# Performance work log

Measured on AMD Instinct MI355X. Metric: run time of the kernel, lower is better.

Reference implementation:

```python
import jax, jax.numpy as jnp
import numpy as np

B, CIN, COUT, K, IH, IW = 2, 32, 32, 9, 256, 256
OH, OW = 512, 512


def setup_inputs() -> dict:
    key = jax.random.key(0)
    k0, k1, k2, k3 = jax.random.split(key, 4)
    stdv = 1.0 / np.sqrt(CIN * K)
    x = jax.random.normal(k0, (B, CIN, IH, IW), jnp.float32)
    weight = jax.random.uniform(k1, (CIN, COUT, K), jnp.float32, -stdv, stdv)
    bias = jax.random.uniform(k2, (COUT,), jnp.float32, -stdv, stdv)
    # continuous (x, y) coords into the OUTPUT plane; keep strictly inside so x0+1/y0+1 are valid
    sm = jax.random.uniform(k3, (IH, IW, K, 2), jnp.float32)
    scale = jnp.array([(OW - 1) * 0.999, (OH - 1) * 0.999], jnp.float32)
    sample_map = sm * scale
    return {"x": x, "weight": weight, "bias": bias, "sample_map": sample_map, "oh": OH, "ow": OW}


def reference(x, weight, bias, sample_map, oh, ow):
    Bb, Cin, Ih, Iw = x.shape
    Cout = weight.shape[1]
    Kk = weight.shape[2]
    P = Ih * Iw
    xf = x.reshape(Bb, Cin, P)
    # per-kernel-tap weight transform of every input pixel: [B, Cout, K, P]
    contrib = jnp.einsum('bip,iok->bokp', xf, weight)

    sx = sample_map[..., 0].reshape(P, Kk).T  # [K, P] x-coords in output
    sy = sample_map[..., 1].reshape(P, Kk).T  # [K, P] y-coords in output
    x0f = jnp.floor(sx)
    y0f = jnp.floor(sy)
    dx = sx - x0f
    dy = sy - y0f
    x0 = jnp.clip(x0f.astype(jnp.int32), 0, ow - 1)
    y0 = jnp.clip(y0f.astype(jnp.int32), 0, oh - 1)
    x1 = jnp.clip(x0 + 1, 0, ow - 1)
    y1 = jnp.clip(y0 + 1, 0, oh - 1)

    # bilinear splat weights and flat output indices for the 4 corners: [4, K, P]
    w = jnp.stack([(1 - dx) * (1 - dy), dx * (1 - dy), (1 - dx) * dy, dx * dy], 0)
    idx = jnp.stack([y0 * ow + x0, y0 * ow + x1, y1 * ow + x0, y1 * ow + x1], 0)

    vals = contrib[:, :, None, :, :] * w[None, None, :, :, :]  # [B, Cout, 4, K, P]
    out = jnp.zeros((Bb, Cout, oh * ow), vals.dtype).at[:, :, idx].add(vals)
    return out.reshape(Bb, Cout, oh, ow) + bias[None, :, None, None]
```

## Files before the change

### kernel.cpp

```cpp
#include <hip/hip_runtime.h>
#include <hip/hip_fp16.h>

#define CIN 32
#define COUT 32
#define KK 9
#define PIX 65536
#define OH 512
#define OW 512
#define OHOW (OH*OW)
#define NCH 64
#define TW 16
#define TH 4
#define TPX (TW*TH)
#define NTX (OW/TW)
#define NTY (OH/TH)
#define NTILE (NTX*NTY)
#define NBIN NTILE
#define NPK (PIX*KK)
#define NSEG 4
#define SCAP 96
#define CAPT (NSEG*SCAP)

#define OFF_CNT 0
#define OFF_WT  (256*1024)
#define OFF_ENT (512*1024)
#define OFF_CB  (OFF_ENT + (size_t)NBIN*NSEG*SCAP*8)
#define WS_NEED (OFF_CB + (size_t)NPK*NCH*2)

typedef __bf16    bf16x8 __attribute__((ext_vector_type(8)));
typedef _Float16  f16x8  __attribute__((ext_vector_type(8)));
typedef float     f32x4  __attribute__((ext_vector_type(4)));

__device__ __forceinline__ unsigned short f2h(float v)
{
    return __half_as_ushort(__float2half_rn(v));
}

__device__ __forceinline__ void corners(float sx, float sy,
    int& x0, int& y0, int& x1, int& y1, float& dx, float& dy)
{
    const float x0f = floorf(sx), y0f = floorf(sy);
    dx = sx - x0f; dy = sy - y0f;
    x0 = min(max((int)x0f, 0), OW - 1);
    y0 = min(max((int)y0f, 0), OH - 1);
    x1 = min(x0 + 1, OW - 1);
    y1 = min(y0 + 1, OH - 1);
}

__global__ __launch_bounds__(256) void k_wtb(
    const float* __restrict__ w, __bf16* __restrict__ wth, __bf16* __restrict__ wtl)
{
    const int t = blockIdx.x * 256 + threadIdx.x;
    if (t < KK * COUT * CIN) {
        const int i = t & 31;
        const int o = (t >> 5) & 31;
        const int k = t >> 10;
        const float v = w[(i * COUT + o) * KK + k];
        const __bf16 h = (__bf16)v;
        wth[t] = h;
        wtl[t] = (__bf16)(v - (float)h);
    }
}

__global__ __launch_bounds__(256, 1) void k_contrib5(
    const float* __restrict__ x, const __bf16* __restrict__ wth,
    const __bf16* __restrict__ wtl, const float* __restrict__ smap,
    unsigned short* __restrict__ cb, unsigned* __restrict__ cnt,
    uint2* __restrict__ ent)
{
    __shared__ __align__(16) unsigned short patch[4][2][16][72];
    const int tid = threadIdx.x, lane = tid & 63;
    const int wu = __builtin_amdgcn_readfirstlane(tid >> 6);
    const int p0 = blockIdx.x * 64;
    const unsigned seg = blockIdx.x & 3;
    const int colp = lane & 15;
    const int q    = lane >> 4;
    const int cig  = q * 8;

    bf16x8 xh[2], xl[2];
    #pragma unroll
    for (int b = 0; b < 2; ++b) {
        const int p = p0 + wu * 16 + colp;
        #pragma unroll
        for (int j = 0; j < 8; ++j) {
            const float v = x[(size_t)(b * 32 + cig + j) * PIX + p];
            const __bf16 h = (__bf16)v;
            xh[b][j] = h;
            xl[b][j] = (__bf16)(v - (float)h);
        }
    }
    bf16x8 wwh[2][2], wwl[2][2];
    #pragma unroll
    for (int oh = 0; oh < 2; ++oh) {
        wwh[0][oh] = *(const bf16x8*)(wth + (oh * 16 + colp) * 32 + cig);
        wwl[0][oh] = *(const bf16x8*)(wtl + (oh * 16 + colp) * 32 + cig);
    }

    unsigned aS[3][4], aA[3][4], aR[3][4], aW[3];
    #pragma unroll
    for (int it = 0; it < 3; ++it) {
        const int idx = tid + it * 256;
        const bool vit = idx < 576;
        const int t = min(p0 * KK + idx, NPK - 1);
        const float sx = smap[2 * t], sy = smap[2 * t + 1];
        int x0, y0, x1, y1; float dx, dy;
        corners(sx, sy, x0, y0, x1, y1, dx, dy);
        const int g0 = x0 >> 4, g1 = x1 >> 4;
        const int t0 = y0 >> 2, t1 = y1 >> 2;
        aW[it] = (unsigned)f2h(dx) | ((unsigned)f2h(dy) << 16);
        const bool dg = (g1 != g0), dt = (t1 != t0);
        const bool cond[4] = { vit, vit && dg, vit && dt, vit && dg && dt };
        const int  tys[4]  = { t0, t0, t1, t1 };
        const int  gss[4]  = { g0, g1, g0, g1 };
        #pragma unroll
        for (int e = 0; e < 4; ++e) {
            unsigned slot = 0xFFFFFFFFu;
            const int bin = tys[e] * 32 + gss[e];
            const unsigned lxb = (unsigned)(x0 - gss[e] * TW + 1);
            const unsigned lyb = (unsigned)(y0 - tys[e] * TH + 1);
            if (cond[e]) slot = atomicAdd(&cnt[seg * NBIN + bin], 1u);
            aS[it][e] = slot;
            aA[it][e] = ((unsigned)bin * NSEG + seg) * SCAP;
            aR[it][e] = (unsigned)t | (lxb << 20) | (lyb << 25);
        }
    }

    const int pxr = lane >> 2, cc = lane & 3;
    #pragma unroll
    for (int k = 0; k < KK; ++k) {
        const int kb = k & 1;
        const int cur = k & 1, nxt = cur ^ 1;
        if (k + 1 < KK) {
            const __bf16* wb = wth + (k + 1) * (COUT * CIN);
            const __bf16* lb = wtl + (k + 1) * (COUT * CIN);
            #pragma unroll
            for (int oh = 0; oh < 2; ++oh) {
                wwh[nxt][oh] = *(const bf16x8*)(wb + (oh * 16 + colp) * 32 + cig);
                wwl[nxt][oh] = *(const bf16x8*)(lb + (oh * 16 + colp) * 32 + cig);
            }
        }
        #pragma unroll
        for (int cg = 0; cg < 4; ++cg) {
            const int b = cg >> 1, oh = cg & 1;
            f32x4 a = {0.f, 0.f, 0.f, 0.f};
            a = __builtin_amdgcn_mfma_f32_16x16x32_bf16(wwh[cur][oh], xh[b], a, 0, 0, 0);
            a = __builtin_amdgcn_mfma_f32_16x16x32_bf16(wwl[cur][oh], xh[b], a, 0, 0, 0);
            a = __builtin_amdgcn_mfma_f32_16x16x32_bf16(wwh[cur][oh], xl[b], a, 0, 0, 0);
            const unsigned d0 = (unsigned)f2h(a[0]) | ((unsigned)f2h(a[1]) << 16);
            const unsigned d1 = (unsigned)f2h(a[2]) | ((unsigned)f2h(a[3]) << 16);
            *(uint2*)&patch[wu][kb][colp][cg * 16 + q * 4] = make_uint2(d0, d1);
        }
        const uint4 a0 = *(const uint4*)&patch[wu][kb][pxr][cc * 8];
        const uint4 a1 = *(const uint4*)&patch[wu][kb][pxr][32 + cc * 8];
        unsigned short* dst = cb + (size_t)(p0 + wu * 16 + pxr) * 576 + k * 64 + cc * 8;
        *(uint4*)dst        = a0;
        *(uint4*)(dst + 32) = a1;
    }

    #pragma unroll
    for (int it = 0; it < 3; ++it) {
        #pragma unroll
        for (int e = 0; e < 4; ++e) {
            if (aS[it][e] < SCAP)
                ent[(size_t)aA[it][e] + aS[it][e]] = make_uint2(aR[it][e], aW[it]);
        }
    }
}

__global__ __launch_bounds__(256, 4) void k_gather(
    const unsigned short* __restrict__ cb, const uint2* __restrict__ ent,
    const unsigned* __restrict__ cnt, const float* __restrict__ bias,
    float* __restrict__ out)
{
    __shared__ __align__(16) unsigned char smem[32768];
    __shared__ __align__(16) uint2 elist[CAPT];
    const int tid = threadIdx.x, lane = tid & 63;
    const int wv = __builtin_amdgcn_readfirstlane(tid >> 6);
    const int bt = blockIdx.x;
    const int tx0 = (bt & 31) * TW;
    const int ty0 = (bt >> 5) * TH;

    const unsigned c0 = min(cnt[0 * NBIN + bt], (unsigned)SCAP);
    const unsigned c1 = min(cnt[1 * NBIN + bt], (unsigned)SCAP);
    const unsigned c2 = min(cnt[2 * NBIN + bt], (unsigned)SCAP);
    const unsigned c3 = min(cnt[3 * NBIN + bt], (unsigned)SCAP);
    const unsigned o1 = c0, o2 = c0 + c1, o3 = o2 + c2;
    const unsigned count = o3 + c3;
    {
        const uint2* e0 = ent + ((size_t)bt * NSEG + 0) * SCAP;
        const uint2* e1 = ent + ((size_t)bt * NSEG + 1) * SCAP;
        const uint2* e2 = ent + ((size_t)bt * NSEG + 2) * SCAP;
        const uint2* e3 = ent + ((size_t)bt * NSEG + 3) * SCAP;
        if ((unsigned)tid < c0) elist[tid]      = e0[tid];
        if ((unsigned)tid < c1) elist[o1 + tid] = e1[tid];
        if ((unsigned)tid < c2) elist[o2 + tid] = e2[tid];
        if ((unsigned)tid < c3) elist[o3 + tid] = e3[tid];
    }
    __syncthreads();

    const int nb = (int)(count + 63) >> 6;

    f32x4 acc[4] = {{0.f,0.f,0.f,0.f},{0.f,0.f,0.f,0.f},
                    {0.f,0.f,0.f,0.f},{0.f,0.f,0.f,0.f}};

    for (int it = 0; it <= nb; ++it) {
        const int bb = it & 1;
        unsigned short* Wb = (unsigned short*)(smem + bb * 8192);
        unsigned short* Cv = (unsigned short*)(smem + 16384 + bb * 8192);
        if (it < nb) {
            uint4* wq = (uint4*)Wb;
            const uint4 z = make_uint4(0u, 0u, 0u, 0u);
            wq[tid] = z; wq[tid + 256] = z;
        }
        __syncthreads();

        unsigned short u[16];
        if (it < nb) {
            {
                const int eL = tid >> 2, cn = tid & 3;
                const unsigned idx = (unsigned)(it * 64 + eL);
                if (idx < count) {
                    const uint2 r = elist[idx];
                    const int lx = (int)((r.x >> 20) & 31) - 1 + (cn & 1);
                    const int ly = (int)((r.x >> 25) & 7) - 1 + (cn >> 1);
                    if (((unsigned)lx < TW) & ((unsigned)ly < TH)) {
                        const float dx = __half2float(__ushort_as_half((unsigned short)(r.y & 0xFFFF)));
                        const float dy = __half2float(__ushort_as_half((unsigned short)(r.y >> 16)));
                        const float wx = (cn & 1) ? dx : 1.f - dx;
                        const float wy = (cn >> 1) ? dy : 1.f - dy;
                        const int px = ly * TW + lx;
                        Wb[px * 64 + (eL ^ ((px & 7) << 3))] = f2h(wx * wy);
                    }
                }
            }
            #pragma unroll
            for (int j = 0; j < 16; ++j) {
                const unsigned idx = (unsigned)(it * 64 + wv * 16 + j);
                unsigned short v = 0;
                if (idx < count) {
                    const unsigned row = elist[idx].x & 0xFFFFFu;
                    v = cb[((size_t)row << 6) + lane];
                }
                u[j] = v;
            }
        }
        if (it > 0) {
            const int pb = bb ^ 1;
            const unsigned short* Wp = (const unsigned short*)(smem + pb * 8192);
            const unsigned short* Cp = (const unsigned short*)(smem + 16384 + pb * 8192);
            const int m = lane & 15, kh = lane >> 4;
            const int px = wv * 16 + m;
            f16x8 af[2];
            #pragma unroll
            for (int kc = 0; kc < 2; ++kc)
                af[kc] = *(const f16x8*)(Wp + px * 64 + (((kc * 4 + kh) ^ (px & 7)) << 3));
            #pragma unroll
            for (int n = 0; n < 4; ++n) {
                const int ch = n * 16 + m;
                #pragma unroll
                for (int kc = 0; kc < 2; ++kc) {
                    const f16x8 bf = *(const f16x8*)(Cp + ch * 64 + (((kc * 4 + kh) ^ (ch & 7)) << 3));
                    acc[n] = __builtin_amdgcn_mfma_f32_16x16x32_f16(af[kc], bf, acc[n], 0, 0, 0);
                }
            }
        }
        if (it < nb) {
            uint4* cvq = (uint4*)Cv;
            const uint4 pk0 = make_uint4(
                (unsigned)u[0]  | ((unsigned)u[1]  << 16),
                (unsigned)u[2]  | ((unsigned)u[3]  << 16),
                (unsigned)u[4]  | ((unsigned)u[5]  << 16),
                (unsigned)u[6]  | ((unsigned)u[7]  << 16));
            const uint4 pk1 = make_uint4(
                (unsigned)u[8]  | ((unsigned)u[9]  << 16),
                (unsigned)u[10] | ((unsigned)u[11] << 16),
                (unsigned)u[12] | ((unsigned)u[13] << 16),
                (unsigned)u[14] | ((unsigned)u[15] << 16));
            cvq[lane * 8 + ((wv * 2)     ^ (lane & 7))] = pk0;
            cvq[lane * 8 + ((wv * 2 + 1) ^ (lane & 7))] = pk1;
        }
        __syncthreads();
    }

    float* stage = (float*)smem;
    #pragma unroll
    for (int n = 0; n < 4; ++n) {
        #pragma unroll
        for (int r = 0; r < 4; ++r)
            stage[(wv * 16 + (lane >> 4) * 4 + r) * 65 + n * 16 + (lane & 15)] = acc[n][r];
    }
    __syncthreads();
    const int py = lane >> 4, pxx = lane & 15;
    const size_t q = (size_t)(ty0 + py) * OW + tx0 + pxx;
    #pragma unroll
    for (int j = 0; j < 16; ++j) {
        const int c = wv * 16 + j;
        out[(size_t)c * OHOW + q] = stage[(py * 16 + pxx) * 65 + c] + bias[c & 31];
    }
}

__global__ __launch_bounds__(576) void mtc_scatter_direct(
    const float* __restrict__ x, const float* __restrict__ weight,
    const float* __restrict__ smap, float* __restrict__ acc)
{
    __shared__ float xs[64][68];
    __shared__ float sm[64 * KK * 2];
    const int t = threadIdx.x;
    const int p0 = blockIdx.x * 64;
    if (t < 512) {
        const int pp = t & 63, c0 = t >> 6;
        #pragma unroll
        for (int ch = 0; ch < 8; ++ch) {
            const int c = c0 + ch * 8;
            xs[pp][c] = x[(size_t)c * PIX + p0 + pp];
        }
    }
    for (int i = t; i < 64 * KK * 2; i += 576)
        sm[i] = smap[(size_t)p0 * (KK * 2) + i];
    const int k = t >> 6, lane = t & 63, b = lane >> 5, o = lane & 31;
    float wreg[CIN];
    #pragma unroll
    for (int i = 0; i < CIN; ++i) wreg[i] = weight[(i * COUT + o) * KK + k];
    __syncthreads();
    for (int pp = 0; pp < 64; ++pp) {
        const float sx = sm[(pp * KK + k) * 2], sy = sm[(pp * KK + k) * 2 + 1];
        int x0, y0, x1, y1; float dx, dy;
        corners(sx, sy, x0, y0, x1, y1, dx, dy);
        const float* xrow = &xs[pp][b * 32];
        float cv = 0.f;
        #pragma unroll
        for (int j = 0; j < 8; ++j) {
            const float4 xv = *(const float4*)(xrow + 4 * j);
            cv += xv.x * wreg[4*j] + xv.y * wreg[4*j+1] + xv.z * wreg[4*j+2] + xv.w * wreg[4*j+3];
        }
        const size_t base = (size_t)lane * OHOW;
        atomicAdd(&acc[base + y0 * OW + x0], cv * (1.f - dx) * (1.f - dy));
        atomicAdd(&acc[base + y0 * OW + x1], cv * dx * (1.f - dy));
        atomicAdd(&acc[base + y1 * OW + x0], cv * (1.f - dx) * dy);
        atomicAdd(&acc[base + y1 * OW + x1], cv * dx * dy);
    }
}

__global__ __launch_bounds__(256) void mtc_bias_add(
    float* __restrict__ out, const float* __restrict__ bias)
{
    const size_t i = (size_t)blockIdx.x * 256 + threadIdx.x;
    out[i] += bias[(i >> 18) & 31];
}

extern "C" void kernel_launch(void* const* d_in, const int* in_sizes, int n_in,
                              void* d_out, int out_size, void* d_ws, size_t ws_size,
                              hipStream_t stream) {
    const float* x      = (const float*)d_in[0];
    const float* weight = (const float*)d_in[1];
    const float* bias   = (const float*)d_in[2];
    const float* smap   = (const float*)d_in[3];
    float* out = (float*)d_out;
    char* ws = (char*)d_ws;

    if (ws_size >= WS_NEED) {
        unsigned* cnt = (unsigned*)(ws + OFF_CNT);
        __bf16* wth   = (__bf16*)(ws + OFF_WT);
        __bf16* wtl   = wth + KK * COUT * CIN;
        uint2* ent    = (uint2*)(ws + OFF_ENT);
        unsigned short* cb = (unsigned short*)(ws + OFF_CB);

        hipMemsetAsync(cnt, 0, NSEG * NBIN * sizeof(unsigned), stream);
        k_wtb<<<(KK * COUT * CIN + 255) / 256, 256, 0, stream>>>(weight, wth, wtl);
        k_contrib5<<<PIX / 64, 256, 0, stream>>>(x, wth, wtl, smap, cb, cnt, ent);
        k_gather<<<NTILE, 256, 0, stream>>>(cb, ent, cnt, bias, out);
    } else {
        hipMemsetAsync(out, 0, (size_t)OHOW * NCH * sizeof(float), stream);
        mtc_scatter_direct<<<PIX / 64, 576, 0, stream>>>(x, weight, smap, out);
        mtc_bias_add<<<(OHOW * NCH) / 256, 256, 0, stream>>>(out, bias);
    }
}
```

Measured before the change: 169.5 us.

## Prefetch first four gather batches up front and fuse counter reset into init kernel

The gather kernel drops its double-buffered LDS loop. It now issues the global cb loads for the first four batches of 64 entries up front into registers, then processes each batch with a single LDS buffer, which halves LDS use and removes the occupancy hint from launch bounds. The memset of the bin counters is folded into the weight-conversion kernel (renamed k_init) to save one launch. This adds register pressure from the four 16-element prefetch arrays and more barriers per batch, in exchange for more memory-level parallelism on the irregular gathers.

```diff
diff --git a/kernel.cpp b/kernel.cpp
--- a/kernel.cpp
+++ b/kernel.cpp
@@ -47,10 +47,12 @@
     y1 = min(y0 + 1, OH - 1);
 }
 
-__global__ __launch_bounds__(256) void k_wtb(
-    const float* __restrict__ w, __bf16* __restrict__ wth, __bf16* __restrict__ wtl)
+__global__ __launch_bounds__(256) void k_init(
+    const float* __restrict__ w, __bf16* __restrict__ wth,
+    __bf16* __restrict__ wtl, unsigned* __restrict__ cnt)
 {
     const int t = blockIdx.x * 256 + threadIdx.x;
+    if (t < NSEG * NBIN) cnt[t] = 0;
     if (t < KK * COUT * CIN) {
         const int i = t & 31;
         const int o = (t >> 5) & 31;
@@ -140,15 +142,15 @@
             }
         }
         #pragma unroll
-        for (int cg = 0; cg < 4; ++cg) {
-            const int b = cg >> 1, oh = cg & 1;
+        for (int cg_ = 0; cg_ < 4; ++cg_) {
+            const int b = cg_ >> 1, oh = cg_ & 1;
             f32x4 a = {0.f, 0.f, 0.f, 0.f};
             a = __builtin_amdgcn_mfma_f32_16x16x32_bf16(wwh[cur][oh], xh[b], a, 0, 0, 0);
             a = __builtin_amdgcn_mfma_f32_16x16x32_bf16(wwl[cur][oh], xh[b], a, 0, 0, 0);
             a = __builtin_amdgcn_mfma_f32_16x16x32_bf16(wwh[cur][oh], xl[b], a, 0, 0, 0);
             const unsigned d0 = (unsigned)f2h(a[0]) | ((unsigned)f2h(a[1]) << 16);
             const unsigned d1 = (unsigned)f2h(a[2]) | ((unsigned)f2h(a[3]) << 16);
-            *(uint2*)&patch[wu][kb][colp][cg * 16 + q * 4] = make_uint2(d0, d1);
+            *(uint2*)&patch[wu][kb][colp][cg_ * 16 + q * 4] = make_uint2(d0, d1);
         }
         const uint4 a0 = *(const uint4*)&patch[wu][kb][pxr][cc * 8];
         const uint4 a1 = *(const uint4*)&patch[wu][kb][pxr][32 + cc * 8];
@@ -167,13 +169,66 @@
     }
 }
 
-__global__ __launch_bounds__(256, 4) void k_gather(
+#define LOADU(UU, ITb) { \
+    _Pragma("unroll") \
+    for (int j = 0; j < 16; ++j) { \
+        const unsigned idx = (unsigned)((ITb) * 64 + wv * 16 + j); \
+        unsigned short v = 0; \
+        if (idx < count) \
+            v = cb[((size_t)(elist[idx].x & 0xFFFFFu) << 6) + lane]; \
+        UU[j] = v; \
+    } }
+
+#define BATCH_BODY(ITc, UU) { \
+    { uint4* wq = (uint4*)Wb; const uint4 z = make_uint4(0u,0u,0u,0u); \
+      wq[tid] = z; wq[tid + 256] = z; } \
+    __syncthreads(); \
+    { const int eL = tid >> 2, cn = tid & 3; \
+      const unsigned idx = (unsigned)((ITc) * 64 + eL); \
+      if (idx < count) { \
+        const uint2 r = elist[idx]; \
+        const int lx = (int)((r.x >> 20) & 31) - 1 + (cn & 1); \
+        const int ly = (int)((r.x >> 25) & 7) - 1 + (cn >> 1); \
+        if (((unsigned)lx < TW) & ((unsigned)ly < TH)) { \
+            const float dx = __half2float(__ushort_as_half((unsigned short)(r.y & 0xFFFF))); \
+            const float dy = __half2float(__ushort_as_half((unsigned short)(r.y >> 16))); \
+            const float wx = (cn & 1) ? dx : 1.f - dx; \
+            const float wy = (cn >> 1) ? dy : 1.f - dy; \
+            const int px = ly * TW + lx; \
+            Wb[px * 64 + (eL ^ ((px & 7) << 3))] = f2h(wx * wy); \
+        } } } \
+    { uint4* cvq = (uint4*)Cv; \
+      const uint4 pk0 = make_uint4( \
+        (unsigned)UU[0]  | ((unsigned)UU[1]  << 16), (unsigned)UU[2]  | ((unsigned)UU[3]  << 16), \
+        (unsigned)UU[4]  | ((unsigned)UU[5]  << 16), (unsigned)UU[6]  | ((unsigned)UU[7]  << 16)); \
+      const uint4 pk1 = make_uint4( \
+        (unsigned)UU[8]  | ((unsigned)UU[9]  << 16), (unsigned)UU[10] | ((unsigned)UU[11] << 16), \
+        (unsigned)UU[12] | ((unsigned)UU[13] << 16), (unsigned)UU[14] | ((unsigned)UU[15] << 16)); \
+      cvq[lane * 8 + ((wv * 2)     ^ (lane & 7))] = pk0; \
+      cvq[lane * 8 + ((wv * 2 + 1) ^ (lane & 7))] = pk1; } \
+    __syncthreads(); \
+    { const int m = lane & 15, kh = lane >> 4; \
+      const int px = wv * 16 + m; \
+      const f16x8 af0 = *(const f16x8*)(Wb + px * 64 + ((kh       ^ (px & 7)) << 3)); \
+      const f16x8 af1 = *(const f16x8*)(Wb + px * 64 + (((4 + kh) ^ (px & 7)) << 3)); \
+      _Pragma("unroll") \
+      for (int n = 0; n < 4; ++n) { \
+        const int ch = n * 16 + m; \
+        const f16x8 bf0 = *(const f16x8*)(Cv + ch * 64 + ((kh       ^ (ch & 7)) << 3)); \
+        acc[n] = __builtin_amdgcn_mfma_f32_16x16x32_f16(af0, bf0, acc[n], 0, 0, 0); \
+        const f16x8 bf1 = *(const f16x8*)(Cv + ch * 64 + (((4 + kh) ^ (ch & 7)) << 3)); \
+        acc[n] = __builtin_amdgcn_mfma_f32_16x16x32_f16(af1, bf1, acc[n], 0, 0, 0); } } \
+    __syncthreads(); }
+
+__global__ __launch_bounds__(256) void k_gather(
     const unsigned short* __restrict__ cb, const uint2* __restrict__ ent,
     const unsigned* __restrict__ cnt, const float* __restrict__ bias,
     float* __restrict__ out)
 {
-    __shared__ __align__(16) unsigned char smem[32768];
+    __shared__ __align__(16) unsigned char smem[16640];
     __shared__ __align__(16) uint2 elist[CAPT];
+    unsigned short* Wb = (unsigned short*)smem;
+    unsigned short* Cv = (unsigned short*)(smem + 8192);
     const int tid = threadIdx.x, lane = tid & 63;
     const int wv = __builtin_amdgcn_readfirstlane(tid >> 6);
     const int bt = blockIdx.x;
@@ -200,86 +255,20 @@
 
     const int nb = (int)(count + 63) >> 6;
 
+    unsigned short uA[16], uB[16], uC[16], uD[16];
+    LOADU(uA, 0); LOADU(uB, 1); LOADU(uC, 2); LOADU(uD, 3);
+
     f32x4 acc[4] = {{0.f,0.f,0.f,0.f},{0.f,0.f,0.f,0.f},
                     {0.f,0.f,0.f,0.f},{0.f,0.f,0.f,0.f}};
 
-    for (int it = 0; it <= nb; ++it) {
-        const int bb = it & 1;
-        unsigned short* Wb = (unsigned short*)(smem + bb * 8192);
-        unsigned short* Cv = (unsigned short*)(smem + 16384 + bb * 8192);
-        if (it < nb) {
-            uint4* wq = (uint4*)Wb;
-            const uint4 z = make_uint4(0u, 0u, 0u, 0u);
-            wq[tid] = z; wq[tid + 256] = z;
-        }
-        __syncthreads();
-
-        unsigned short u[16];
-        if (it < nb) {
-            {
-                const int eL = tid >> 2, cn = tid & 3;
-                const unsigned idx = (unsigned)(it * 64 + eL);
-                if (idx < count) {
-                    const uint2 r = elist[idx];
-                    const int lx = (int)((r.x >> 20) & 31) - 1 + (cn & 1);
-                    const int ly = (int)((r.x >> 25) & 7) - 1 + (cn >> 1);
-                    if (((unsigned)lx < TW) & ((unsigned)ly < TH)) {
-                        const float dx = __half2float(__ushort_as_half((unsigned short)(r.y & 0xFFFF)));
-                        const float dy = __half2float(__ushort_as_half((unsigned short)(r.y >> 16)));
-                        const float wx = (cn & 1) ? dx : 1.f - dx;
-                        const float wy = (cn >> 1) ? dy : 1.f - dy;
-                        const int px = ly * TW + lx;
-                        Wb[px * 64 + (eL ^ ((px & 7) << 3))] = f2h(wx * wy);
-                    }
-                }
-            }
-            #pragma unroll
-            for (int j = 0; j < 16; ++j) {
-                const unsigned idx = (unsigned)(it * 64 + wv * 16 + j);
-                unsigned short v = 0;
-                if (idx < count) {
-                    const unsigned row = elist[idx].x & 0xFFFFFu;
-                    v = cb[((size_t)row << 6) + lane];
-                }
-                u[j] = v;
-            }
-        }
-        if (it > 0) {
-            const int pb = bb ^ 1;
-            const unsigned short* Wp = (const unsigned short*)(smem + pb * 8192);
-            const unsigned short* Cp = (const unsigned short*)(smem + 16384 + pb * 8192);
-            const int m = lane & 15, kh = lane >> 4;
-            const int px = wv * 16 + m;
-            f16x8 af[2];
-            #pragma unroll
-            for (int kc = 0; kc < 2; ++kc)
-                af[kc] = *(const f16x8*)(Wp + px * 64 + (((kc * 4 + kh) ^ (px & 7)) << 3));
-            #pragma unroll
-            for (int n = 0; n < 4; ++n) {
-                const int ch = n * 16 + m;
-                #pragma unroll
-                for (int kc = 0; kc < 2; ++kc) {
-                    const f16x8 bf = *(const f16x8*)(Cp + ch * 64 + (((kc * 4 + kh) ^ (ch & 7)) << 3));
-                    acc[n] = __builtin_amdgcn_mfma_f32_16x16x32_f16(af[kc], bf, acc[n], 0, 0, 0);
-                }
-            }
-        }
-        if (it < nb) {
-            uint4* cvq = (uint4*)Cv;
-            const uint4 pk0 = make_uint4(
-                (unsigned)u[0]  | ((unsigned)u[1]  << 16),
-                (unsigned)u[2]  | ((unsigned)u[3]  << 16),
-                (unsigned)u[4]  | ((unsigned)u[5]  << 16),
-                (unsigned)u[6]  | ((unsigned)u[7]  << 16));
-            const uint4 pk1 = make_uint4(
-                (unsigned)u[8]  | ((unsigned)u[9]  << 16),
-                (unsigned)u[10] | ((unsigned)u[11] << 16),
-                (unsigned)u[12] | ((unsigned)u[13] << 16),
-                (unsigned)u[14] | ((unsigned)u[15] << 16));
-            cvq[lane * 8 + ((wv * 2)     ^ (lane & 7))] = pk0;
-            cvq[lane * 8 + ((wv * 2 + 1) ^ (lane & 7))] = pk1;
-        }
-        __syncthreads();
+    if (0 < nb) { BATCH_BODY(0, uA); }
+    if (1 < nb) { BATCH_BODY(1, uB); }
+    if (2 < nb) { BATCH_BODY(2, uC); }
+    if (3 < nb) { BATCH_BODY(3, uD); }
+    for (int it = 4; it < nb; ++it) {
+        unsigned short ut[16];
+        LOADU(ut, it);
+        BATCH_BODY(it, ut);
     }
 
     float* stage = (float*)smem;
@@ -291,11 +280,11 @@
     }
     __syncthreads();
     const int py = lane >> 4, pxx = lane & 15;
-    const size_t q = (size_t)(ty0 + py) * OW + tx0 + pxx;
+    const size_t qq = (size_t)(ty0 + py) * OW + tx0 + pxx;
     #pragma unroll
     for (int j = 0; j < 16; ++j) {
         const int c = wv * 16 + j;
-        out[(size_t)c * OHOW + q] = stage[(py * 16 + pxx) * 65 + c] + bias[c & 31];
+        out[(size_t)c * OHOW + qq] = stage[(py * 16 + pxx) * 65 + c] + bias[c & 31];
     }
 }
 
@@ -365,8 +354,7 @@
         uint2* ent    = (uint2*)(ws + OFF_ENT);
         unsigned short* cb = (unsigned short*)(ws + OFF_CB);
 
-        hipMemsetAsync(cnt, 0, NSEG * NBIN * sizeof(unsigned), stream);
-        k_wtb<<<(KK * COUT * CIN + 255) / 256, 256, 0, stream>>>(weight, wth, wtl);
+        k_init<<<64, 256, 0, stream>>>(weight, wth, wtl, cnt);
         k_contrib5<<<PIX / 64, 256, 0, stream>>>(x, wth, wtl, smap, cb, cnt, ent);
         k_gather<<<NTILE, 256, 0, stream>>>(cb, ent, cnt, bias, out);
     } else {
```

Result: no change. 166.9 us (-1.5%).
